# Optimization experiments

Hardware: AMD Instinct MI355X
Metric: run time of the kernel (lower is better)

The kernel has to match this reference:

```python
import jax, jax.numpy as jnp
import numpy as np

D_MODEL, N_HEADS, RANK = 1024, 16, 32
HEAD_DIM = D_MODEL // N_HEADS
B, S = 4, 2048


def setup_inputs() -> dict:
    key = jax.random.key(0)
    ks = jax.random.split(key, 8)
    inp = {
        "x": jax.random.normal(ks[0], (B, S, D_MODEL), dtype=jnp.float32),
        "mask": jnp.ones((B, S), dtype=jnp.int32),
        "qkv_u": jax.random.normal(ks[1], (D_MODEL, RANK), jnp.float32) / D_MODEL ** 0.5,
        "qkv_v": jax.random.normal(ks[2], (RANK, 3 * D_MODEL), jnp.float32) / RANK ** 0.5,
        "qkv_b": jnp.zeros((3 * D_MODEL,), jnp.float32),
        "u_attn": jax.random.normal(ks[3], (N_HEADS, HEAD_DIM, RANK), jnp.float32) / HEAD_DIM ** 0.5,
        "v_attn": jax.random.normal(ks[4], (N_HEADS, RANK, HEAD_DIM), jnp.float32) / RANK ** 0.5,
        "out_u": jax.random.normal(ks[5], (D_MODEL, RANK), jnp.float32) / D_MODEL ** 0.5,
        "out_v": jax.random.normal(ks[6], (RANK, D_MODEL), jnp.float32) / RANK ** 0.5,
        "out_b": jnp.zeros((D_MODEL,), jnp.float32),
    }
    return inp


def reference(x, mask, qkv_u, qkv_v, qkv_b, u_attn, v_attn, out_u, out_v, out_b):
    bs, seq_len, d_model = x.shape
    n_heads, head_dim, rank = u_attn.shape
    scale = 1.0 / jnp.sqrt(jnp.float32(rank))

    # Low-rank QKV projection: [B,S,3D]
    qkv = (x @ qkv_u) @ qkv_v + qkv_b
    q, k, v = jnp.split(qkv, 3, axis=-1)

    def to_heads(t):  # [B,S,D] -> [B,H,S,hd]
        return t.reshape(bs, seq_len, n_heads, head_dim).transpose(0, 2, 1, 3)

    q, k, v = to_heads(q), to_heads(k), to_heads(v)

    # Rank-projected Q/K: [B,H,S,r]
    q_low = jnp.einsum("bhsd,hdr->bhsr", q, u_attn)
    k_low = jnp.einsum("bhtd,hdr->bhtr", k, u_attn)
    scores = jnp.einsum("bhsr,bhtr->bhst", q_low, k_low) * scale

    # mask: [B,S] keys; masked_fill where mask == 0
    scores = jnp.where(mask[:, None, None, :] == 0, jnp.float32(-jnp.inf), scores)
    attn = jax.nn.softmax(scores, axis=-1)  # dropout is identity in eval

    v_low = jnp.einsum("bhtd,hdr->bhtr", v, u_attn)
    context_low = jnp.einsum("bhst,bhtr->bhsr", attn, v_low)
    context = jnp.einsum("bhsr,hrd->bhsd", context_low, v_attn)
    context = context.transpose(0, 2, 1, 3).reshape(bs, seq_len, d_model)

    return (context @ out_u) @ out_v + out_b
```

## Files before the change

kernel.cpp:

```cpp
#include <hip/hip_runtime.h>
#include <hip/hip_bf16.h>

typedef unsigned int u32;
typedef unsigned short u16;
typedef __attribute__((ext_vector_type(8))) __bf16 bf16x8;
typedef __attribute__((ext_vector_type(16))) float f32x16;
typedef __attribute__((ext_vector_type(2))) unsigned int u32x2;

#define QSCALE 0.25505418f
#define MFMA __builtin_amdgcn_mfma_f32_32x32x16_bf16


static __device__ __forceinline__ u16 f2b(float f) {
  __hip_bfloat16 h = __float2bfloat16(f);
  return *reinterpret_cast<u16*>(&h);
}
static __device__ __forceinline__ u32 cvtpk(float lo, float hi) {
  u32 r;
  asm("v_cvt_pk_bf16_f32 %0, %1, %2" : "=v"(r) : "v"(lo), "v"(hi));
  return r;
}

static __device__ __forceinline__ float xhalf_sum(float v) {
#if __has_builtin(__builtin_amdgcn_permlane32_swap)
  u32 a = __float_as_uint(v);
  u32x2 r = __builtin_amdgcn_permlane32_swap(a, a, false, false);
  return __uint_as_float(r[0]) + __uint_as_float(r[1]);
#else
  return v + __shfl_xor(v, 32);
#endif
}

static __device__ __forceinline__ int tau(int p) {
  int g = p >> 2;
  int gk = (g & 4) | ((g & 1) << 1) | ((g >> 1) & 1);
  return (gk << 2) | (p & 3);
}

static __device__ __forceinline__ int fmoff(int row, int col) {
  return (col >> 4) * 512 + (((col >> 3) & 1) * 32 + (row & 31)) * 8 + (col & 7);
}

__global__ __launch_bounds__(256) void k_prep(const float* __restrict__ qkv_v,
                                              const float* __restrict__ qkv_b,
                                              const float* __restrict__ u_attn,
                                              const float* __restrict__ v_attn,
                                              const float* __restrict__ out_u,
                                              const float* __restrict__ qkv_u,
                                              const float* __restrict__ out_v,
                                              const int* __restrict__ mask,
                                              u16* __restrict__ WQF, u16* __restrict__ WKF,
                                              u16* __restrict__ WVF, float* __restrict__ BQKV,
                                              u16* __restrict__ WOTF, u16* __restrict__ UTF,
                                              u16* __restrict__ OVF, int* __restrict__ flag) {
  __shared__ int mred[4];
  int blk = blockIdx.x;
  int tid = threadIdx.x;
  if (blk < 16) {
    int h = blk;
    int r = tid & 31, g = tid >> 5;
    for (int rp = g; rp < 32; rp += 8) {
      float aq = 0.f, ak = 0.f, av = 0.f;
      for (int d = 0; d < 64; ++d) {
        float u = u_attn[(h * 64 + d) * 32 + r];
        aq += qkv_v[rp * 3072 + h * 64 + d] * u;
        ak += qkv_v[rp * 3072 + 1024 + h * 64 + d] * u;
        av += qkv_v[rp * 3072 + 2048 + h * 64 + d] * u;
      }
      int o = h * 1024 + fmoff(r, rp);
      WQF[o] = f2b(aq);
      WKF[o] = f2b(ak);
      WVF[o] = f2b(av);
    }
    for (int rr = g; rr < 32; rr += 8) {
      float a = 0.f;
      for (int d = 0; d < 64; ++d)
        a += v_attn[(h * 32 + rr) * 64 + d] * out_u[(h * 64 + d) * 32 + r];
      WOTF[fmoff(r, h * 32 + rr)] = f2b(a);
    }
    if (tid < 32) {
      float aq = 0.f, ak = 0.f, av = 0.f;
      for (int d = 0; d < 64; ++d) {
        float u = u_attn[(h * 64 + d) * 32 + r];
        aq += qkv_b[h * 64 + d] * u;
        ak += qkv_b[1024 + h * 64 + d] * u;
        av += qkv_b[2048 + h * 64 + d] * u;
      }
      BQKV[h * 32 + r] = aq;
      BQKV[512 + h * 32 + r] = ak;
      BQKV[1024 + h * 32 + r] = av;
    }
  } else if (blk < 24) {
    int kb = (blk - 16) * 128;
    for (int i = tid; i < 4096; i += 256) {
      int r = i >> 7, kl = i & 127;
      int k = kb + kl;
      UTF[fmoff(r, k)] = f2b(qkv_u[k * 32 + r]);
    }
  } else if (blk < 32) {
    int db = (blk - 24) * 128;
    for (int i = tid; i < 4096; i += 256) {
      int dl = i >> 5, r = i & 31;
      int d = db + dl;
      OVF[(d >> 5) * 1024 + fmoff(d, r)] = f2b(out_v[r * 1024 + d]);
    }
  } else {
    int mall = 1;
    for (int i = tid; i < 8192; i += 256) mall &= (mask[i] != 0) ? 1 : 0;
    int wa = __all(mall) ? 1 : 0;
    if ((tid & 63) == 0) mred[tid >> 6] = wa;
    __syncthreads();
    if (tid == 0) flag[0] = mred[0] & mred[1] & mred[2] & mred[3];
  }
}

__global__ __launch_bounds__(512) void k_proj(const float* __restrict__ x,
                                              const u16* __restrict__ UTF,
                                              u16* __restrict__ TF) {
  __shared__ float xl[2][32][129];
  __shared__ float red[8][32][33];
  int tid = threadIdx.x;
  int w = tid >> 6, l = tid & 63, lo = l & 31, hi = l >> 5;
  int m0 = blockIdx.x * 32;
  int srow = tid >> 4, scol = (tid & 15) * 8;
  const float* xp = x + (size_t)(m0 + srow) * 1024 + scol;
  float4 r0 = *(const float4*)(xp);
  float4 r1 = *(const float4*)(xp + 4);
  xp += 128;
  f32x16 acc = {};
  for (int ch = 0; ch < 8; ++ch) {
    int buf = ch & 1;
    float* dst = &xl[buf][srow][scol];
    dst[0] = r0.x; dst[1] = r0.y; dst[2] = r0.z; dst[3] = r0.w;
    dst[4] = r1.x; dst[5] = r1.y; dst[6] = r1.z; dst[7] = r1.w;
    if (ch < 7) {
      r0 = *(const float4*)(xp);
      r1 = *(const float4*)(xp + 4);
      xp += 128;
    }
    __syncthreads();
    const float* src = &xl[buf][lo][w * 16 + hi * 8];
    union { bf16x8 v; u32 u[4]; } af;
    af.u[0] = cvtpk(src[0], src[1]);
    af.u[1] = cvtpk(src[2], src[3]);
    af.u[2] = cvtpk(src[4], src[5]);
    af.u[3] = cvtpk(src[6], src[7]);
    bf16x8 bf = *(const bf16x8*)(UTF + (ch * 8 + w) * 512 + l * 8);
    acc = MFMA(af.v, bf, acc, 0, 0, 0);
  }
#pragma unroll
  for (int i = 0; i < 16; ++i)
    red[w][(i & 3) + 8 * (i >> 2) + 4 * hi][lo] = acc[i];
  __syncthreads();
  int m = tid >> 4, c = (tid & 15) * 2;
  float v0 = 0.f, v1 = 0.f;
#pragma unroll
  for (int ww = 0; ww < 8; ++ww) {
    v0 += red[ww][m][c + 0];
    v1 += red[ww][m][c + 1];
  }
  *(u32*)(TF + (size_t)blockIdx.x * 1024 + fmoff(m, c)) = cvtpk(v0, v1);
}

__global__ __launch_bounds__(256) void k_lowproj(const u16* __restrict__ TF,
                                                 const u16* __restrict__ WQF,
                                                 const u16* __restrict__ WKF,
                                                 const u16* __restrict__ WVF,
                                                 const float* __restrict__ BQKV,
                                                 u16* __restrict__ QLF, u16* __restrict__ KF,
                                                 u16* __restrict__ VF) {
  __shared__ float vtf[32][132];
  int tid = threadIdx.x;
  int w = tid >> 6, l = tid & 63, lo = l & 31, hi = l >> 5;
  int blk = blockIdx.x;
  int bh = blk >> 4, sb = (blk & 15) * 128;
  int b = bh >> 4, h = bh & 15;
  int qt = (sb >> 5) + w;

  const u16* wq = WQF + h * 1024 + l * 8;
  const u16* wk = WKF + h * 1024 + l * 8;
  const u16* wv = WVF + h * 1024 + l * 8;
  bf16x8 aq0 = *(const bf16x8*)(wq), aq1 = *(const bf16x8*)(wq + 512);
  bf16x8 ak0 = *(const bf16x8*)(wk), ak1 = *(const bf16x8*)(wk + 512);
  bf16x8 av0 = *(const bf16x8*)(wv), av1 = *(const bf16x8*)(wv + 512);

  const u16* tp = TF + (size_t)(b * 64 + qt) * 1024 + l * 8;
  bf16x8 tb0 = *(const bf16x8*)(tp), tb1 = *(const bf16x8*)(tp + 512);

  f32x16 cq = {}, ck = {}, cv = {};
  cq = MFMA(aq0, tb0, cq, 0, 0, 0);
  cq = MFMA(aq1, tb1, cq, 0, 0, 0);
  ck = MFMA(ak0, tb0, ck, 0, 0, 0);
  ck = MFMA(ak1, tb1, ck, 0, 0, 0);
  cv = MFMA(av0, tb0, cv, 0, 0, 0);
  cv = MFMA(av1, tb1, cv, 0, 0, 0);

  size_t qbase = (size_t)bh * 65536 + (size_t)qt * 1024;
  size_t tbase = (size_t)bh * 65536 + (size_t)qt * 1024;
  int slp = w * 32 + tau(lo);
#pragma unroll
  for (int g2 = 0; g2 < 4; ++g2) {
    float4 bq4 = *(const float4*)(BQKV + h * 32 + g2 * 8 + 4 * hi);
    float4 bk4 = *(const float4*)(BQKV + 512 + h * 32 + g2 * 8 + 4 * hi);
    float4 bv4 = *(const float4*)(BQKV + 1024 + h * 32 + g2 * 8 + 4 * hi);
    float q0 = (cq[4 * g2 + 0] + bq4.x) * QSCALE;
    float q1 = (cq[4 * g2 + 1] + bq4.y) * QSCALE;
    float q2 = (cq[4 * g2 + 2] + bq4.z) * QSCALE;
    float q3 = (cq[4 * g2 + 3] + bq4.w) * QSCALE;
    uint2 qo; qo.x = cvtpk(q0, q1); qo.y = cvtpk(q2, q3);
    *(uint2*)(QLF + qbase + (g2 >> 1) * 512 + ((g2 & 1) * 32 + lo) * 8 + 4 * hi) = qo;
    uint2 ko;
    ko.x = cvtpk(ck[4 * g2 + 0] + bk4.x, ck[4 * g2 + 1] + bk4.y);
    ko.y = cvtpk(ck[4 * g2 + 2] + bk4.z, ck[4 * g2 + 3] + bk4.w);
    *(uint2*)(KF + tbase + (g2 >> 1) * 512 + (g2 & 1) * 256 + lo * 8 + 4 * hi) = ko;
    int rbase = g2 * 8 + 4 * hi;
    vtf[rbase + 0][slp] = cv[4 * g2 + 0] + bv4.x;
    vtf[rbase + 1][slp] = cv[4 * g2 + 1] + bv4.y;
    vtf[rbase + 2][slp] = cv[4 * g2 + 2] + bv4.z;
    vtf[rbase + 3][slp] = cv[4 * g2 + 3] + bv4.w;
  }
  __syncthreads();
  for (int u = tid; u < 512; u += 256) {
    int r = u >> 4, su = (u & 15) * 8;
    const float* src = &vtf[r][su];
    uint4 o;
    o.x = cvtpk(src[0], src[1]);
    o.y = cvtpk(src[2], src[3]);
    o.z = cvtpk(src[4], src[5]);
    o.w = cvtpk(src[6], src[7]);
    int c = su & 31, tloc = su >> 5;
    *(uint4*)(VF + (size_t)bh * 65536 + (size_t)((sb >> 5) + tloc) * 1024 +
              (c >> 4) * 512 + ((c >> 3) & 1) * 256 + r * 8) = o;
  }
}

__global__ __launch_bounds__(256) void k_attn(const u16* __restrict__ QLF,
                                              const u16* __restrict__ KF,
                                              const u16* __restrict__ VF,
                                              const int* __restrict__ mask,
                                              const int* __restrict__ flag,
                                              u16* __restrict__ CTX2) {
  __shared__ float pacc[2][64][17];
  __shared__ float pl[2][64];
  __shared__ u32 cls[64][17];
  int tid = threadIdx.x;
  int wave = tid >> 6, l = tid & 63, lo = l & 31, hi = l >> 5;
  int blk = blockIdx.x;
  int xcd = blk & 7, slot = blk >> 3;
  int bh = xcd * 8 + (slot >> 5);
  int qpair = slot & 31;
  int qi = wave & 1;
  int khalf = wave >> 1;
  int qt = qpair * 2 + qi;
  int b = bh >> 4, h = bh & 15;

  const u16* qp = QLF + (size_t)bh * 65536 + (size_t)qt * 1024 + l * 8;
  bf16x8 qb0 = *(const bf16x8*)(qp);
  bf16x8 qb1 = *(const bf16x8*)(qp + 512);

  size_t fbase = (size_t)bh * 65536 + (size_t)khalf * 32768 + l * 8;
  const u16* kp = KF + fbase;
  const u16* vp = VF + fbase;

  f32x16 acc = {};
  float l_run = 0.f;

  if (flag[0]) {
#pragma unroll 1
    for (int kt = 0; kt < 32; ++kt) {
      bf16x8 ka0 = *(const bf16x8*)(kp);
      bf16x8 ka1 = *(const bf16x8*)(kp + 512);
      kp += 1024;
      f32x16 sc = {};
      sc = MFMA(ka0, qb0, sc, 0, 0, 0);
      sc = MFMA(ka1, qb1, sc, 0, 0, 0);
      bf16x8 va0 = *(const bf16x8*)(vp);
      bf16x8 va1 = *(const bf16x8*)(vp + 512);
      vp += 1024;
      union { bf16x8 v; u32 u[4]; } fa;
      float a0 = __builtin_amdgcn_exp2f(sc[0]);
      float a1 = __builtin_amdgcn_exp2f(sc[1]);
      float a2 = __builtin_amdgcn_exp2f(sc[2]);
      float a3 = __builtin_amdgcn_exp2f(sc[3]);
      fa.u[0] = cvtpk(a0, a1);
      fa.u[1] = cvtpk(a2, a3);
      float t0 = (a0 + a1) + (a2 + a3);
      a0 = __builtin_amdgcn_exp2f(sc[4]);
      a1 = __builtin_amdgcn_exp2f(sc[5]);
      a2 = __builtin_amdgcn_exp2f(sc[6]);
      a3 = __builtin_amdgcn_exp2f(sc[7]);
      fa.u[2] = cvtpk(a0, a1);
      fa.u[3] = cvtpk(a2, a3);
      float t1 = (a0 + a1) + (a2 + a3);
      acc = MFMA(va0, fa.v, acc, 0, 0, 0);
      union { bf16x8 v; u32 u[4]; } fc;
      a0 = __builtin_amdgcn_exp2f(sc[8]);
      a1 = __builtin_amdgcn_exp2f(sc[9]);
      a2 = __builtin_amdgcn_exp2f(sc[10]);
      a3 = __builtin_amdgcn_exp2f(sc[11]);
      fc.u[0] = cvtpk(a0, a1);
      fc.u[1] = cvtpk(a2, a3);
      float t2 = (a0 + a1) + (a2 + a3);
      a0 = __builtin_amdgcn_exp2f(sc[12]);
      a1 = __builtin_amdgcn_exp2f(sc[13]);
      a2 = __builtin_amdgcn_exp2f(sc[14]);
      a3 = __builtin_amdgcn_exp2f(sc[15]);
      fc.u[2] = cvtpk(a0, a1);
      fc.u[3] = cvtpk(a2, a3);
      float t3 = (a0 + a1) + (a2 + a3);
      acc = MFMA(va1, fc.v, acc, 0, 0, 0);
      l_run += (t0 + t1) + (t2 + t3);
    }
  } else {
    const int* mp = mask + b * 2048 + khalf * 1024 + lo;
#pragma unroll 1
    for (int kt = 0; kt < 32; ++kt) {
      unsigned long long bm = __ballot(mp[0] != 0);
      mp += 32;
      bf16x8 ka0 = *(const bf16x8*)(kp);
      bf16x8 ka1 = *(const bf16x8*)(kp + 512);
      kp += 1024;
      f32x16 sc = {};
      sc = MFMA(ka0, qb0, sc, 0, 0, 0);
      sc = MFMA(ka1, qb1, sc, 0, 0, 0);
      u32 km = (u32)bm;
#pragma unroll
      for (int i = 0; i < 16; ++i) {
        int key = (i & 3) + 8 * (i >> 2) + 4 * hi;
        if (!((km >> key) & 1)) sc[i] = -3.0e38f;
      }
      bf16x8 va0 = *(const bf16x8*)(vp);
      bf16x8 va1 = *(const bf16x8*)(vp + 512);
      vp += 1024;
      union { bf16x8 v; u32 u[4]; } fa;
      float a0 = __builtin_amdgcn_exp2f(sc[0]);
      float a1 = __builtin_amdgcn_exp2f(sc[1]);
      float a2 = __builtin_amdgcn_exp2f(sc[2]);
      float a3 = __builtin_amdgcn_exp2f(sc[3]);
      fa.u[0] = cvtpk(a0, a1);
      fa.u[1] = cvtpk(a2, a3);
      float t0 = (a0 + a1) + (a2 + a3);
      a0 = __builtin_amdgcn_exp2f(sc[4]);
      a1 = __builtin_amdgcn_exp2f(sc[5]);
      a2 = __builtin_amdgcn_exp2f(sc[6]);
      a3 = __builtin_amdgcn_exp2f(sc[7]);
      fa.u[2] = cvtpk(a0, a1);
      fa.u[3] = cvtpk(a2, a3);
      float t1 = (a0 + a1) + (a2 + a3);
      acc = MFMA(va0, fa.v, acc, 0, 0, 0);
      union { bf16x8 v; u32 u[4]; } fc;
      a0 = __builtin_amdgcn_exp2f(sc[8]);
      a1 = __builtin_amdgcn_exp2f(sc[9]);
      a2 = __builtin_amdgcn_exp2f(sc[10]);
      a3 = __builtin_amdgcn_exp2f(sc[11]);
      fc.u[0] = cvtpk(a0, a1);
      fc.u[1] = cvtpk(a2, a3);
      float t2 = (a0 + a1) + (a2 + a3);
      a0 = __builtin_amdgcn_exp2f(sc[12]);
      a1 = __builtin_amdgcn_exp2f(sc[13]);
      a2 = __builtin_amdgcn_exp2f(sc[14]);
      a3 = __builtin_amdgcn_exp2f(sc[15]);
      fc.u[2] = cvtpk(a0, a1);
      fc.u[3] = cvtpk(a2, a3);
      float t3 = (a0 + a1) + (a2 + a3);
      acc = MFMA(va1, fc.v, acc, 0, 0, 0);
      l_run += (t0 + t1) + (t2 + t3);
    }
  }

  if (khalf) {
#pragma unroll
    for (int i = 0; i < 16; ++i) pacc[qi][l][i] = acc[i];
    pl[qi][l] = l_run;
  }
  __syncthreads();
  if (!khalf) {
#pragma unroll
    for (int i = 0; i < 16; ++i) acc[i] += pacc[qi][l][i];
    l_run += pl[qi][l];
    l_run = xhalf_sum(l_run);
    float inv = 1.0f / l_run;
    int qloc = qi * 32 + lo;
#pragma unroll
    for (int g2 = 0; g2 < 4; ++g2) {
      cls[qloc][g2 * 4 + 2 * hi] = cvtpk(acc[4 * g2 + 0] * inv, acc[4 * g2 + 1] * inv);
      cls[qloc][g2 * 4 + 2 * hi + 1] = cvtpk(acc[4 * g2 + 2] * inv, acc[4 * g2 + 3] * inv);
    }
  }
  __syncthreads();
  int st2 = tid >> 7, kcl = (tid >> 6) & 1, lw = tid & 63;
  const u32* src = &cls[st2 * 32 + (lw & 31)][kcl * 8 + (lw >> 5) * 4];
  uint4 v0;
  v0.x = src[0]; v0.y = src[1]; v0.z = src[2]; v0.w = src[3];
  *(uint4*)(CTX2 + (size_t)(b * 64 + qpair * 2 + st2) * 16384 +
            (2 * h + kcl) * 512 + lw * 8) = v0;
}

__global__ __launch_bounds__(512) void k_epi1(const u16* __restrict__ CTX2,
                                              const u16* __restrict__ WOTF,
                                              u16* __restrict__ YLF) {
  __shared__ float red[8][32][33];
  int tid = threadIdx.x;
  int w = tid >> 6, l = tid & 63, lo = l & 31, hi = l >> 5;
  int stile = blockIdx.x;
  const u16* cp = CTX2 + (size_t)stile * 16384 + (4 * w) * 512 + l * 8;
  const u16* wp = WOTF + (4 * w) * 512 + l * 8;
  f32x16 acc = {};
  for (int st = 0; st < 4; ++st) {
    bf16x8 a = *(const bf16x8*)(cp);
    bf16x8 bb = *(const bf16x8*)(wp);
    cp += 512;
    wp += 512;
    acc = MFMA(a, bb, acc, 0, 0, 0);
  }
#pragma unroll
  for (int i = 0; i < 16; ++i)
    red[w][(i & 3) + 8 * (i >> 2) + 4 * hi][lo] = acc[i];
  __syncthreads();
  int m = tid >> 4, c = (tid & 15) * 2;
  float v0 = 0.f, v1 = 0.f;
#pragma unroll
  for (int ww = 0; ww < 8; ++ww) {
    v0 += red[ww][m][c + 0];
    v1 += red[ww][m][c + 1];
  }
  *(u32*)(YLF + (size_t)stile * 1024 + fmoff(m, c)) = cvtpk(v0, v1);
}

__global__ __launch_bounds__(256) void k_epi2(const u16* __restrict__ YLF,
                                              const u16* __restrict__ OVF,
                                              const float* __restrict__ out_b,
                                              float* __restrict__ out) {
  __shared__ float ol[32][133];
  int tid = threadIdx.x;
  int w = tid >> 6, l = tid & 63, lo = l & 31, hi = l >> 5;
  int blk = blockIdx.x;
  int stile = blk >> 3;
  int s0 = stile * 32;
  int d0 = (blk & 7) * 128;
  int dtile = (blk & 7) * 4 + w;
  const u16* ap = OVF + (size_t)dtile * 1024 + l * 8;
  bf16x8 a0 = *(const bf16x8*)(ap), a1 = *(const bf16x8*)(ap + 512);
  const u16* bp = YLF + (size_t)stile * 1024 + l * 8;
  bf16x8 b0 = *(const bf16x8*)(bp), b1 = *(const bf16x8*)(bp + 512);
  f32x16 acc = {};
  acc = MFMA(a0, b0, acc, 0, 0, 0);
  acc = MFMA(a1, b1, acc, 0, 0, 0);
#pragma unroll
  for (int i = 0; i < 16; ++i)
    ol[lo][w * 32 + (i & 3) + 8 * (i >> 2) + 4 * hi] = acc[i];
  __syncthreads();
  for (int u = tid; u < 1024; u += 256) {
    int s = u >> 5, c = (u & 31) * 4;
    float4 ob = *(const float4*)(out_b + d0 + c);
    float4 o;
    o.x = ol[s][c + 0] + ob.x;
    o.y = ol[s][c + 1] + ob.y;
    o.z = ol[s][c + 2] + ob.z;
    o.w = ol[s][c + 3] + ob.w;
    *(float4*)(out + (size_t)(s0 + s) * 1024 + d0 + c) = o;
  }
}

extern "C" void kernel_launch(void* const* d_in, const int* in_sizes, int n_in,
                              void* d_out, int out_size, void* d_ws, size_t ws_size,
                              hipStream_t stream) {
  const float* x = (const float*)d_in[0];
  const int* mask = (const int*)d_in[1];
  const float* qkv_u = (const float*)d_in[2];
  const float* qkv_v = (const float*)d_in[3];
  const float* qkv_b = (const float*)d_in[4];
  const float* u_attn = (const float*)d_in[5];
  const float* v_attn = (const float*)d_in[6];
  const float* out_u = (const float*)d_in[7];
  const float* out_v = (const float*)d_in[8];
  const float* out_b = (const float*)d_in[9];
  float* out = (float*)d_out;

  char* w = (char*)d_ws;
  u16* WQF = (u16*)(w + 0);
  u16* WKF = (u16*)(w + (32 << 10));
  u16* WVF = (u16*)(w + (64 << 10));
  float* BQ = (float*)(w + (96 << 10));
  int* FLAG = (int*)(w + (102 << 10));
  u16* WOTF = (u16*)(w + (104 << 10));
  u16* UTF = (u16*)(w + (136 << 10));
  u16* OVF = (u16*)(w + (200 << 10));
  u16* TF = (u16*)(w + (1 << 20));
  u16* QLF = (u16*)(w + (2 << 20));
  u16* KF = (u16*)(w + (10 << 20));
  u16* VF = (u16*)(w + (18 << 20));
  u16* CTX2 = (u16*)(w + (26 << 20));
  u16* YLF = (u16*)(w + (34 << 20));

  k_prep<<<33, 256, 0, stream>>>(qkv_v, qkv_b, u_attn, v_attn, out_u, qkv_u, out_v,
                                 mask, WQF, WKF, WVF, BQ, WOTF, UTF, OVF, FLAG);
  k_proj<<<256, 512, 0, stream>>>(x, UTF, TF);
  k_lowproj<<<1024, 256, 0, stream>>>(TF, WQF, WKF, WVF, BQ, QLF, KF, VF);
  k_attn<<<2048, 256, 0, stream>>>(QLF, KF, VF, mask, FLAG, CTX2);
  k_epi1<<<256, 512, 0, stream>>>(CTX2, WOTF, YLF);
  k_epi2<<<2048, 256, 0, stream>>>(YLF, OVF, out_b, out);
}
```

Measured before the change: 112.0 us.

## Fuse projection with low-rank QKV and merge both epilogue kernels

Merges k_proj and k_lowproj into one kernel. Each 512-thread block computes a 32-row rank-32 tile in shared memory and then expands it to Q/K/V for all 16 heads, two heads per wave. Likewise merges k_epi1 and k_epi2 so each block computes its low-rank context tile and writes all 1024 output columns in four passes. This removes two launches and the TF/YLF global round trips. In exchange, the QKV and output expansion run on only 256 blocks instead of 1024 and 2048, which lowers parallelism for those stages and adds extra syncs.

```diff
diff --git a/kernel.cpp b/kernel.cpp
--- a/kernel.cpp
+++ b/kernel.cpp
@@ -114,123 +114,120 @@
   }
 }
 
-__global__ __launch_bounds__(512) void k_proj(const float* __restrict__ x,
-                                              const u16* __restrict__ UTF,
-                                              u16* __restrict__ TF) {
-  __shared__ float xl[2][32][129];
-  __shared__ float red[8][32][33];
-  int tid = threadIdx.x;
-  int w = tid >> 6, l = tid & 63, lo = l & 31, hi = l >> 5;
-  int m0 = blockIdx.x * 32;
-  int srow = tid >> 4, scol = (tid & 15) * 8;
-  const float* xp = x + (size_t)(m0 + srow) * 1024 + scol;
-  float4 r0 = *(const float4*)(xp);
-  float4 r1 = *(const float4*)(xp + 4);
-  xp += 128;
-  f32x16 acc = {};
-  for (int ch = 0; ch < 8; ++ch) {
-    int buf = ch & 1;
-    float* dst = &xl[buf][srow][scol];
-    dst[0] = r0.x; dst[1] = r0.y; dst[2] = r0.z; dst[3] = r0.w;
-    dst[4] = r1.x; dst[5] = r1.y; dst[6] = r1.z; dst[7] = r1.w;
-    if (ch < 7) {
-      r0 = *(const float4*)(xp);
-      r1 = *(const float4*)(xp + 4);
-      xp += 128;
-    }
-    __syncthreads();
-    const float* src = &xl[buf][lo][w * 16 + hi * 8];
-    union { bf16x8 v; u32 u[4]; } af;
-    af.u[0] = cvtpk(src[0], src[1]);
-    af.u[1] = cvtpk(src[2], src[3]);
-    af.u[2] = cvtpk(src[4], src[5]);
-    af.u[3] = cvtpk(src[6], src[7]);
-    bf16x8 bf = *(const bf16x8*)(UTF + (ch * 8 + w) * 512 + l * 8);
-    acc = MFMA(af.v, bf, acc, 0, 0, 0);
-  }
-#pragma unroll
-  for (int i = 0; i < 16; ++i)
-    red[w][(i & 3) + 8 * (i >> 2) + 4 * hi][lo] = acc[i];
-  __syncthreads();
-  int m = tid >> 4, c = (tid & 15) * 2;
-  float v0 = 0.f, v1 = 0.f;
-#pragma unroll
-  for (int ww = 0; ww < 8; ++ww) {
-    v0 += red[ww][m][c + 0];
-    v1 += red[ww][m][c + 1];
-  }
-  *(u32*)(TF + (size_t)blockIdx.x * 1024 + fmoff(m, c)) = cvtpk(v0, v1);
-}
-
-__global__ __launch_bounds__(256) void k_lowproj(const u16* __restrict__ TF,
+__global__ __launch_bounds__(512) void k_projlow(const float* __restrict__ x,
+                                                 const u16* __restrict__ UTF,
                                                  const u16* __restrict__ WQF,
                                                  const u16* __restrict__ WKF,
                                                  const u16* __restrict__ WVF,
                                                  const float* __restrict__ BQKV,
                                                  u16* __restrict__ QLF, u16* __restrict__ KF,
                                                  u16* __restrict__ VF) {
-  __shared__ float vtf[32][132];
+  __shared__ float xl[2][32][129];
+  __shared__ float red[8][32][33];
   int tid = threadIdx.x;
   int w = tid >> 6, l = tid & 63, lo = l & 31, hi = l >> 5;
-  int blk = blockIdx.x;
-  int bh = blk >> 4, sb = (blk & 15) * 128;
-  int b = bh >> 4, h = bh & 15;
-  int qt = (sb >> 5) + w;
-
-  const u16* wq = WQF + h * 1024 + l * 8;
-  const u16* wk = WKF + h * 1024 + l * 8;
-  const u16* wv = WVF + h * 1024 + l * 8;
-  bf16x8 aq0 = *(const bf16x8*)(wq), aq1 = *(const bf16x8*)(wq + 512);
-  bf16x8 ak0 = *(const bf16x8*)(wk), ak1 = *(const bf16x8*)(wk + 512);
-  bf16x8 av0 = *(const bf16x8*)(wv), av1 = *(const bf16x8*)(wv + 512);
-
-  const u16* tp = TF + (size_t)(b * 64 + qt) * 1024 + l * 8;
-  bf16x8 tb0 = *(const bf16x8*)(tp), tb1 = *(const bf16x8*)(tp + 512);
-
-  f32x16 cq = {}, ck = {}, cv = {};
-  cq = MFMA(aq0, tb0, cq, 0, 0, 0);
-  cq = MFMA(aq1, tb1, cq, 0, 0, 0);
-  ck = MFMA(ak0, tb0, ck, 0, 0, 0);
-  ck = MFMA(ak1, tb1, ck, 0, 0, 0);
-  cv = MFMA(av0, tb0, cv, 0, 0, 0);
-  cv = MFMA(av1, tb1, cv, 0, 0, 0);
-
-  size_t qbase = (size_t)bh * 65536 + (size_t)qt * 1024;
-  size_t tbase = (size_t)bh * 65536 + (size_t)qt * 1024;
-  int slp = w * 32 + tau(lo);
-#pragma unroll
-  for (int g2 = 0; g2 < 4; ++g2) {
-    float4 bq4 = *(const float4*)(BQKV + h * 32 + g2 * 8 + 4 * hi);
-    float4 bk4 = *(const float4*)(BQKV + 512 + h * 32 + g2 * 8 + 4 * hi);
-    float4 bv4 = *(const float4*)(BQKV + 1024 + h * 32 + g2 * 8 + 4 * hi);
-    float q0 = (cq[4 * g2 + 0] + bq4.x) * QSCALE;
-    float q1 = (cq[4 * g2 + 1] + bq4.y) * QSCALE;
-    float q2 = (cq[4 * g2 + 2] + bq4.z) * QSCALE;
-    float q3 = (cq[4 * g2 + 3] + bq4.w) * QSCALE;
-    uint2 qo; qo.x = cvtpk(q0, q1); qo.y = cvtpk(q2, q3);
-    *(uint2*)(QLF + qbase + (g2 >> 1) * 512 + ((g2 & 1) * 32 + lo) * 8 + 4 * hi) = qo;
-    uint2 ko;
-    ko.x = cvtpk(ck[4 * g2 + 0] + bk4.x, ck[4 * g2 + 1] + bk4.y);
-    ko.y = cvtpk(ck[4 * g2 + 2] + bk4.z, ck[4 * g2 + 3] + bk4.w);
-    *(uint2*)(KF + tbase + (g2 >> 1) * 512 + (g2 & 1) * 256 + lo * 8 + 4 * hi) = ko;
-    int rbase = g2 * 8 + 4 * hi;
-    vtf[rbase + 0][slp] = cv[4 * g2 + 0] + bv4.x;
-    vtf[rbase + 1][slp] = cv[4 * g2 + 1] + bv4.y;
-    vtf[rbase + 2][slp] = cv[4 * g2 + 2] + bv4.z;
-    vtf[rbase + 3][slp] = cv[4 * g2 + 3] + bv4.w;
+  int stile = blockIdx.x;
+  int b = stile >> 6, qt = stile & 63;
+  int m0 = stile * 32;
+
+  {
+    int srow = tid >> 4, scol = (tid & 15) * 8;
+    const float* xp = x + (size_t)(m0 + srow) * 1024 + scol;
+    float4 r0 = *(const float4*)(xp);
+    float4 r1 = *(const float4*)(xp + 4);
+    xp += 128;
+    f32x16 acc = {};
+    for (int ch = 0; ch < 8; ++ch) {
+      int buf = ch & 1;
+      float* dst = &xl[buf][srow][scol];
+      dst[0] = r0.x; dst[1] = r0.y; dst[2] = r0.z; dst[3] = r0.w;
+      dst[4] = r1.x; dst[5] = r1.y; dst[6] = r1.z; dst[7] = r1.w;
+      if (ch < 7) {
+        r0 = *(const float4*)(xp);
+        r1 = *(const float4*)(xp + 4);
+        xp += 128;
+      }
+      __syncthreads();
+      const float* src = &xl[buf][lo][w * 16 + hi * 8];
+      union { bf16x8 v; u32 u[4]; } af;
+      af.u[0] = cvtpk(src[0], src[1]);
+      af.u[1] = cvtpk(src[2], src[3]);
+      af.u[2] = cvtpk(src[4], src[5]);
+      af.u[3] = cvtpk(src[6], src[7]);
+      bf16x8 bf = *(const bf16x8*)(UTF + (ch * 8 + w) * 512 + l * 8);
+      acc = MFMA(af.v, bf, acc, 0, 0, 0);
+    }
+#pragma unroll
+    for (int i = 0; i < 16; ++i)
+      red[w][(i & 3) + 8 * (i >> 2) + 4 * hi][lo] = acc[i];
   }
   __syncthreads();
-  for (int u = tid; u < 512; u += 256) {
-    int r = u >> 4, su = (u & 15) * 8;
-    const float* src = &vtf[r][su];
-    uint4 o;
-    o.x = cvtpk(src[0], src[1]);
-    o.y = cvtpk(src[2], src[3]);
-    o.z = cvtpk(src[4], src[5]);
-    o.w = cvtpk(src[6], src[7]);
-    int c = su & 31, tloc = su >> 5;
-    *(uint4*)(VF + (size_t)bh * 65536 + (size_t)((sb >> 5) + tloc) * 1024 +
-              (c >> 4) * 512 + ((c >> 3) & 1) * 256 + r * 8) = o;
+  u16* tl = (u16*)&xl[0][0][0];
+  {
+    int m = tid >> 4, c = (tid & 15) * 2;
+    float v0 = 0.f, v1 = 0.f;
+#pragma unroll
+    for (int ww = 0; ww < 8; ++ww) {
+      v0 += red[ww][m][c + 0];
+      v1 += red[ww][m][c + 1];
+    }
+    *(u32*)(tl + fmoff(m, c)) = cvtpk(v0, v1);
+  }
+  __syncthreads();
+
+  bf16x8 tb0 = *(const bf16x8*)(tl + l * 8);
+  bf16x8 tb1 = *(const bf16x8*)(tl + 512 + l * 8);
+  for (int hh = 0; hh < 2; ++hh) {
+    int h = w * 2 + hh;
+    int bh = b * 16 + h;
+    const u16* wq = WQF + h * 1024 + l * 8;
+    const u16* wk = WKF + h * 1024 + l * 8;
+    const u16* wv = WVF + h * 1024 + l * 8;
+    bf16x8 aq0 = *(const bf16x8*)(wq), aq1 = *(const bf16x8*)(wq + 512);
+    bf16x8 ak0 = *(const bf16x8*)(wk), ak1 = *(const bf16x8*)(wk + 512);
+    bf16x8 av0 = *(const bf16x8*)(wv), av1 = *(const bf16x8*)(wv + 512);
+
+    f32x16 cq = {}, ck = {}, cv = {};
+    cq = MFMA(aq0, tb0, cq, 0, 0, 0);
+    cq = MFMA(aq1, tb1, cq, 0, 0, 0);
+    ck = MFMA(ak0, tb0, ck, 0, 0, 0);
+    ck = MFMA(ak1, tb1, ck, 0, 0, 0);
+    cv = MFMA(av0, tb0, cv, 0, 0, 0);
+    cv = MFMA(av1, tb1, cv, 0, 0, 0);
+
+    size_t base = (size_t)bh * 65536 + (size_t)qt * 1024;
+    int slp = tau(lo);
+#pragma unroll
+    for (int g2 = 0; g2 < 4; ++g2) {
+      float4 bq4 = *(const float4*)(BQKV + h * 32 + g2 * 8 + 4 * hi);
+      float4 bk4 = *(const float4*)(BQKV + 512 + h * 32 + g2 * 8 + 4 * hi);
+      float4 bv4 = *(const float4*)(BQKV + 1024 + h * 32 + g2 * 8 + 4 * hi);
+      float q0 = (cq[4 * g2 + 0] + bq4.x) * QSCALE;
+      float q1 = (cq[4 * g2 + 1] + bq4.y) * QSCALE;
+      float q2 = (cq[4 * g2 + 2] + bq4.z) * QSCALE;
+      float q3 = (cq[4 * g2 + 3] + bq4.w) * QSCALE;
+      uint2 qo; qo.x = cvtpk(q0, q1); qo.y = cvtpk(q2, q3);
+      *(uint2*)(QLF + base + (g2 >> 1) * 512 + ((g2 & 1) * 32 + lo) * 8 + 4 * hi) = qo;
+      uint2 ko;
+      ko.x = cvtpk(ck[4 * g2 + 0] + bk4.x, ck[4 * g2 + 1] + bk4.y);
+      ko.y = cvtpk(ck[4 * g2 + 2] + bk4.z, ck[4 * g2 + 3] + bk4.w);
+      *(uint2*)(KF + base + (g2 >> 1) * 512 + (g2 & 1) * 256 + lo * 8 + 4 * hi) = ko;
+      int rbase = g2 * 8 + 4 * hi;
+      red[w][rbase + 0][slp] = cv[4 * g2 + 0] + bv4.x;
+      red[w][rbase + 1][slp] = cv[4 * g2 + 1] + bv4.y;
+      red[w][rbase + 2][slp] = cv[4 * g2 + 2] + bv4.z;
+      red[w][rbase + 3][slp] = cv[4 * g2 + 3] + bv4.w;
+    }
+    for (int u = l; u < 128; u += 64) {
+      int r = u >> 2, su = (u & 3) * 8;
+      const float* src = &red[w][r][su];
+      uint4 o;
+      o.x = cvtpk(src[0], src[1]);
+      o.y = cvtpk(src[2], src[3]);
+      o.z = cvtpk(src[4], src[5]);
+      o.w = cvtpk(src[6], src[7]);
+      *(uint4*)(VF + base + (su >> 4) * 512 + ((su >> 3) & 1) * 256 + r * 8) = o;
+    }
   }
 }
 
@@ -396,69 +393,73 @@
             (2 * h + kcl) * 512 + lw * 8) = v0;
 }
 
-__global__ __launch_bounds__(512) void k_epi1(const u16* __restrict__ CTX2,
-                                              const u16* __restrict__ WOTF,
-                                              u16* __restrict__ YLF) {
+__global__ __launch_bounds__(512) void k_epi(const u16* __restrict__ CTX2,
+                                             const u16* __restrict__ WOTF,
+                                             const u16* __restrict__ OVF,
+                                             const float* __restrict__ out_b,
+                                             float* __restrict__ out) {
   __shared__ float red[8][32][33];
+  __shared__ u32 yl[32][17];
   int tid = threadIdx.x;
   int w = tid >> 6, l = tid & 63, lo = l & 31, hi = l >> 5;
   int stile = blockIdx.x;
-  const u16* cp = CTX2 + (size_t)stile * 16384 + (4 * w) * 512 + l * 8;
-  const u16* wp = WOTF + (4 * w) * 512 + l * 8;
-  f32x16 acc = {};
-  for (int st = 0; st < 4; ++st) {
-    bf16x8 a = *(const bf16x8*)(cp);
-    bf16x8 bb = *(const bf16x8*)(wp);
-    cp += 512;
-    wp += 512;
-    acc = MFMA(a, bb, acc, 0, 0, 0);
-  }
-#pragma unroll
-  for (int i = 0; i < 16; ++i)
-    red[w][(i & 3) + 8 * (i >> 2) + 4 * hi][lo] = acc[i];
+  int s0 = stile * 32;
+  {
+    const u16* cp = CTX2 + (size_t)stile * 16384 + (4 * w) * 512 + l * 8;
+    const u16* wp = WOTF + (4 * w) * 512 + l * 8;
+    f32x16 acc = {};
+    for (int st = 0; st < 4; ++st) {
+      bf16x8 a = *(const bf16x8*)(cp);
+      bf16x8 bb = *(const bf16x8*)(wp);
+      cp += 512;
+      wp += 512;
+      acc = MFMA(a, bb, acc, 0, 0, 0);
+    }
+#pragma unroll
+    for (int i = 0; i < 16; ++i)
+      red[w][(i & 3) + 8 * (i >> 2) + 4 * hi][lo] = acc[i];
+  }
   __syncthreads();
-  int m = tid >> 4, c = (tid & 15) * 2;
-  float v0 = 0.f, v1 = 0.f;
-#pragma unroll
-  for (int ww = 0; ww < 8; ++ww) {
-    v0 += red[ww][m][c + 0];
-    v1 += red[ww][m][c + 1];
-  }
-  *(u32*)(YLF + (size_t)stile * 1024 + fmoff(m, c)) = cvtpk(v0, v1);
-}
-
-__global__ __launch_bounds__(256) void k_epi2(const u16* __restrict__ YLF,
-                                              const u16* __restrict__ OVF,
-                                              const float* __restrict__ out_b,
-                                              float* __restrict__ out) {
-  __shared__ float ol[32][133];
-  int tid = threadIdx.x;
-  int w = tid >> 6, l = tid & 63, lo = l & 31, hi = l >> 5;
-  int blk = blockIdx.x;
-  int stile = blk >> 3;
-  int s0 = stile * 32;
-  int d0 = (blk & 7) * 128;
-  int dtile = (blk & 7) * 4 + w;
-  const u16* ap = OVF + (size_t)dtile * 1024 + l * 8;
-  bf16x8 a0 = *(const bf16x8*)(ap), a1 = *(const bf16x8*)(ap + 512);
-  const u16* bp = YLF + (size_t)stile * 1024 + l * 8;
-  bf16x8 b0 = *(const bf16x8*)(bp), b1 = *(const bf16x8*)(bp + 512);
-  f32x16 acc = {};
-  acc = MFMA(a0, b0, acc, 0, 0, 0);
-  acc = MFMA(a1, b1, acc, 0, 0, 0);
-#pragma unroll
-  for (int i = 0; i < 16; ++i)
-    ol[lo][w * 32 + (i & 3) + 8 * (i >> 2) + 4 * hi] = acc[i];
+  {
+    int m = tid >> 4, c = (tid & 15) * 2;
+    float v0 = 0.f, v1 = 0.f;
+#pragma unroll
+    for (int ww = 0; ww < 8; ++ww) {
+      v0 += red[ww][m][c + 0];
+      v1 += red[ww][m][c + 1];
+    }
+    yl[m][c >> 1] = cvtpk(v0, v1);
+  }
   __syncthreads();
-  for (int u = tid; u < 1024; u += 256) {
-    int s = u >> 5, c = (u & 31) * 4;
-    float4 ob = *(const float4*)(out_b + d0 + c);
-    float4 o;
-    o.x = ol[s][c + 0] + ob.x;
-    o.y = ol[s][c + 1] + ob.y;
-    o.z = ol[s][c + 2] + ob.z;
-    o.w = ol[s][c + 3] + ob.w;
-    *(float4*)(out + (size_t)(s0 + s) * 1024 + d0 + c) = o;
+  float (*ol)[263] = (float(*)[263])&red[0][0][0];
+  union { bf16x8 v; u32 u[4]; } ub0, ub1;
+#pragma unroll
+  for (int j = 0; j < 4; ++j) {
+    ub0.u[j] = yl[lo][hi * 4 + j];
+    ub1.u[j] = yl[lo][8 + hi * 4 + j];
+  }
+  for (int p = 0; p < 4; ++p) {
+    int dtile = p * 8 + w;
+    const u16* ap = OVF + (size_t)dtile * 1024 + l * 8;
+    bf16x8 a0 = *(const bf16x8*)(ap), a1 = *(const bf16x8*)(ap + 512);
+    f32x16 acc = {};
+    acc = MFMA(a0, ub0.v, acc, 0, 0, 0);
+    acc = MFMA(a1, ub1.v, acc, 0, 0, 0);
+#pragma unroll
+    for (int i = 0; i < 16; ++i)
+      ol[lo][w * 32 + (i & 3) + 8 * (i >> 2) + 4 * hi] = acc[i];
+    __syncthreads();
+    for (int u = tid; u < 2048; u += 512) {
+      int s = u >> 6, c4 = (u & 63) * 4;
+      float4 ob = *(const float4*)(out_b + p * 256 + c4);
+      float4 o;
+      o.x = ol[s][c4 + 0] + ob.x;
+      o.y = ol[s][c4 + 1] + ob.y;
+      o.z = ol[s][c4 + 2] + ob.z;
+      o.w = ol[s][c4 + 3] + ob.w;
+      *(float4*)(out + (size_t)(s0 + s) * 1024 + p * 256 + c4) = o;
+    }
+    __syncthreads();
   }
 }
 
@@ -486,18 +487,14 @@
   u16* WOTF = (u16*)(w + (104 << 10));
   u16* UTF = (u16*)(w + (136 << 10));
   u16* OVF = (u16*)(w + (200 << 10));
-  u16* TF = (u16*)(w + (1 << 20));
   u16* QLF = (u16*)(w + (2 << 20));
   u16* KF = (u16*)(w + (10 << 20));
   u16* VF = (u16*)(w + (18 << 20));
   u16* CTX2 = (u16*)(w + (26 << 20));
-  u16* YLF = (u16*)(w + (34 << 20));
 
   k_prep<<<33, 256, 0, stream>>>(qkv_v, qkv_b, u_attn, v_attn, out_u, qkv_u, out_v,
                                  mask, WQF, WKF, WVF, BQ, WOTF, UTF, OVF, FLAG);
-  k_proj<<<256, 512, 0, stream>>>(x, UTF, TF);
-  k_lowproj<<<1024, 256, 0, stream>>>(TF, WQF, WKF, WVF, BQ, QLF, KF, VF);
+  k_projlow<<<256, 512, 0, stream>>>(x, UTF, WQF, WKF, WVF, BQ, QLF, KF, VF);
   k_attn<<<2048, 256, 0, stream>>>(QLF, KF, VF, mask, FLAG, CTX2);
-  k_epi1<<<256, 512, 0, stream>>>(CTX2, WOTF, YLF);
-  k_epi2<<<2048, 256, 0, stream>>>(YLF, OVF, out_b, out);
-}
+  k_epi<<<256, 512, 0, stream>>>(CTX2, WOTF, OVF, out_b, out);
+}
```

After: 113.6 us. Within noise of the previous version (+1.5%).
